# Kernel optimization log

Measured on AMD Instinct MI355X. Metric: run time of the kernel, lower is better.

## Reference

```python
import jax, jax.numpy as jnp
import numpy as np

MARGIN = 0.3
N, D = 8192, 256
NUM_IDS = 1000


def setup_inputs() -> dict:
    key = jax.random.key(0)
    k1, k2 = jax.random.split(key)
    inputs = jax.random.normal(k1, (N, D), dtype=jnp.float32)
    targets = jax.random.randint(k2, (N,), 0, NUM_IDS, dtype=jnp.int64)
    return {"inputs": inputs, "targets": targets}


def reference(inputs, targets):
    # sim_mat[i, j] = <x_i, x_j>
    sim = jnp.matmul(inputs, inputs.T)  # [n, n]
    same = targets[:, None] == targets[None, :]  # [n, n] bool
    # positives: same label AND sim < 1 (note: strict; diagonal included only if ||x||^2 < 1)
    pos_mask = same & (sim < 1.0)
    # negatives: different label AND sim > margin
    neg_mask = (~same) & (sim > MARGIN)
    pos_loss = jnp.sum(jnp.where(pos_mask, 1.0 - sim, 0.0), axis=1)  # [n]
    neg_loss = jnp.sum(jnp.where(neg_mask, sim, 0.0), axis=1)  # [n]
    n = inputs.shape[0]
    return jnp.sum(pos_loss + neg_loss) / n
```

## Files before the change

kernel.cpp:

```cpp
#include <hip/hip_runtime.h>
#include <hip/hip_bf16.h>


#define MARGINF 0.3f

typedef __attribute__((ext_vector_type(8))) short short8x;
typedef __attribute__((ext_vector_type(16))) float f32x16;

__device__ __forceinline__ unsigned short f2bf(float f) {
    unsigned int u = __float_as_uint(f);
    unsigned int r = (u + 0x7fffu + ((u >> 16) & 1u)) >> 16;
    return (unsigned short)r;
}

__global__ void __launch_bounds__(256) convert_k(const float* __restrict__ x,
                                                 unsigned short* __restrict__ xb) {
    int u = blockIdx.x * 256 + threadIdx.x;
    int lane = u & 63;
    int ks   = (u >> 6) & 15;
    int r32  = u >> 10;
    int row  = r32 * 32 + (lane & 31);
    int col  = ks * 16 + (lane >> 5) * 8;
    const float4* src = reinterpret_cast<const float4*>(x + (size_t)row * 256 + col);
    float4 a = src[0];
    float4 b = src[1];
    short8x o;
    o[0] = (short)f2bf(a.x); o[1] = (short)f2bf(a.y);
    o[2] = (short)f2bf(a.z); o[3] = (short)f2bf(a.w);
    o[4] = (short)f2bf(b.x); o[5] = (short)f2bf(b.y);
    o[6] = (short)f2bf(b.z); o[7] = (short)f2bf(b.w);
    reinterpret_cast<short8x*>(xb)[u] = o;
}

__global__ void __launch_bounds__(256, 3) gemm_loss_k(const unsigned short* __restrict__ xb,
                                                      const int* __restrict__ tg,
                                                      double* __restrict__ partials) {
    const int p = blockIdx.x;
    int bi = (int)(64.5f - sqrtf(64.5f * 64.5f - 2.0f * (float)p));
    if (bi < 0) bi = 0;
    if (bi > 63) bi = 63;
    while (bi > 0 && (bi * (129 - bi)) / 2 > p) --bi;
    while (((bi + 1) * (128 - bi)) / 2 <= p) ++bi;
    const int bj = bi + (p - (bi * (129 - bi)) / 2);

    __shared__ int lti[128];
    __shared__ int ltj[128];
    __shared__ float redbuf[4];

    const int tid  = threadIdx.x;
    const int lane = tid & 63;
    const int wid  = tid >> 6;
    const int wr   = wid >> 1;
    const int wc   = wid & 1;

    if (tid < 128)       lti[tid]        = tg[bi * 128 + tid];
    else                 ltj[tid - 128]  = tg[bj * 128 + (tid - 128)];
    __syncthreads();

    const short8x* xf = reinterpret_cast<const short8x*>(xb);
    const int aIdx = ((bi * 4 + wr * 2) << 10) + lane;
    const int bIdx = ((bj * 4 + wc * 2) << 10) + lane;

    f32x16 acc00 = {}, acc01 = {}, acc10 = {}, acc11 = {};

    short8x a0 = xf[aIdx];
    short8x a1 = xf[aIdx + 1024];
    short8x b0 = xf[bIdx];
    short8x b1 = xf[bIdx + 1024];

#pragma unroll
    for (int ks = 0; ks < 16; ++ks) {
        short8x na0, na1, nb0, nb1;
        if (ks < 15) {
            const int o = (ks + 1) * 64;
            na0 = xf[aIdx + o];
            na1 = xf[aIdx + 1024 + o];
            nb0 = xf[bIdx + o];
            nb1 = xf[bIdx + 1024 + o];
        }
        acc00 = __builtin_amdgcn_mfma_f32_32x32x16_bf16(a0, b0, acc00, 0, 0, 0);
        acc01 = __builtin_amdgcn_mfma_f32_32x32x16_bf16(a0, b1, acc01, 0, 0, 0);
        acc10 = __builtin_amdgcn_mfma_f32_32x32x16_bf16(a1, b0, acc10, 0, 0, 0);
        acc11 = __builtin_amdgcn_mfma_f32_32x32x16_bf16(a1, b1, acc11, 0, 0, 0);
        if (ks < 15) { a0 = na0; a1 = na1; b0 = nb0; b1 = nb1; }
    }

    const int hi4 = (lane >> 5) * 4;
    const int col_l = lane & 31;
    int tjv[2];
#pragma unroll
    for (int fn = 0; fn < 2; ++fn) tjv[fn] = ltj[wc * 64 + fn * 32 + col_l];

    float lsum = 0.f;
    const f32x16* accs[4] = { &acc00, &acc01, &acc10, &acc11 };

    if (bi != bj) {
#pragma unroll
        for (int fm = 0; fm < 2; ++fm) {
#pragma unroll
            for (int fn = 0; fn < 2; ++fn) {
                const f32x16& A = *accs[fm * 2 + fn];
                const int tj = tjv[fn];
#pragma unroll
                for (int r = 0; r < 16; ++r) {
                    const int row_l = (r & 3) + 8 * (r >> 2) + hi4;
                    const int ti = lti[wr * 64 + fm * 32 + row_l];
                    const float s = A[r];
                    const float posv = fmaxf(1.0f - s, 0.0f);
                    const float negv = (s > MARGINF) ? s : 0.0f;
                    lsum += (ti == tj) ? posv : negv;
                }
            }
        }
        lsum *= 2.0f;
    } else {
#pragma unroll
        for (int fm = 0; fm < 2; ++fm) {
#pragma unroll
            for (int fn = 0; fn < 2; ++fn) {
                const f32x16& A = *accs[fm * 2 + fn];
                const int tj = tjv[fn];
                const int cl = wc * 64 + fn * 32 + col_l;
#pragma unroll
                for (int r = 0; r < 16; ++r) {
                    const int row_l = (r & 3) + 8 * (r >> 2) + hi4;
                    const int rl = wr * 64 + fm * 32 + row_l;
                    const int ti = lti[rl];
                    const float s = A[r];
                    const float posv = fmaxf(1.0f - s, 0.0f);
                    const float negv = (s > MARGINF) ? s : 0.0f;
                    const float c = (ti == tj) ? posv : negv;
                    const float w = (cl > rl) ? 2.0f : ((cl == rl) ? 1.0f : 0.0f);
                    lsum += w * c;
                }
            }
        }
    }

#pragma unroll
    for (int mask = 1; mask < 64; mask <<= 1) lsum += __shfl_xor(lsum, mask, 64);
    if (lane == 0) redbuf[wid] = lsum;
    __syncthreads();
    if (tid == 0)
        partials[p] = (double)(redbuf[0] + redbuf[1] + redbuf[2] + redbuf[3]);
}

__global__ void __launch_bounds__(256) finalize_k(const double* __restrict__ partials,
                                                  float* __restrict__ out) {
    double s = 0.0;
    for (int i = threadIdx.x; i < 2080; i += 256) s += partials[i];
#pragma unroll
    for (int mask = 1; mask < 64; mask <<= 1) s += __shfl_xor(s, mask, 64);
    __shared__ double red[4];
    const int wid = threadIdx.x >> 6;
    if ((threadIdx.x & 63) == 0) red[wid] = s;
    __syncthreads();
    if (threadIdx.x == 0)
        out[0] = (float)((red[0] + red[1] + red[2] + red[3]) / 8192.0);
}

extern "C" void kernel_launch(void* const* d_in, const int* in_sizes, int n_in,
                              void* d_out, int out_size, void* d_ws, size_t ws_size,
                              hipStream_t stream) {
    (void)in_sizes; (void)n_in; (void)out_size; (void)ws_size;
    const float* x  = (const float*)d_in[0];
    const int*   tg = (const int*)d_in[1];
    float* out = (float*)d_out;

    double* partials   = (double*)d_ws;
    unsigned short* xb = (unsigned short*)((char*)d_ws + 32768);

    convert_k<<<1024, 256, 0, stream>>>(x, xb);
    gemm_loss_k<<<2080, 256, 0, stream>>>(xb, tg, partials);
    finalize_k<<<1, 256, 0, stream>>>(partials, out);
}
```

Before: 89.26 us.

## Stage GEMM operands through swizzled LDS with triple-buffered async global-to-LDS loads

The GEMM now stages A and B tiles through a three-deep LDS ring buffer using global_load_lds direct copies with an XOR swizzle. Waves read their MFMA fragments from LDS instead of each wave loading its own fragments from global memory in a prepacked layout. The convert kernel is simplified to a plain row-major bf16 conversion. This shares operand loads across waves and overlaps memory with MFMA work, at the cost of 48KB of LDS per block, which may limit the three-blocks-per-CU occupancy, plus extra barriers.

```diff
diff --git a/kernel.cpp b/kernel.cpp
--- a/kernel.cpp
+++ b/kernel.cpp
@@ -15,21 +15,16 @@
 
 __global__ void __launch_bounds__(256) convert_k(const float* __restrict__ x,
                                                  unsigned short* __restrict__ xb) {
-    int u = blockIdx.x * 256 + threadIdx.x;
-    int lane = u & 63;
-    int ks   = (u >> 6) & 15;
-    int r32  = u >> 10;
-    int row  = r32 * 32 + (lane & 31);
-    int col  = ks * 16 + (lane >> 5) * 8;
-    const float4* src = reinterpret_cast<const float4*>(x + (size_t)row * 256 + col);
-    float4 a = src[0];
-    float4 b = src[1];
+    int i = blockIdx.x * 256 + threadIdx.x;
+    const float4* p = reinterpret_cast<const float4*>(x) + (size_t)i * 2;
+    float4 a = p[0];
+    float4 b = p[1];
     short8x o;
     o[0] = (short)f2bf(a.x); o[1] = (short)f2bf(a.y);
     o[2] = (short)f2bf(a.z); o[3] = (short)f2bf(a.w);
     o[4] = (short)f2bf(b.x); o[5] = (short)f2bf(b.y);
     o[6] = (short)f2bf(b.z); o[7] = (short)f2bf(b.w);
-    reinterpret_cast<short8x*>(xb)[u] = o;
+    reinterpret_cast<short8x*>(xb)[i] = o;
 }
 
 __global__ void __launch_bounds__(256, 3) gemm_loss_k(const unsigned short* __restrict__ xb,
@@ -43,6 +38,7 @@
     while (((bi + 1) * (128 - bi)) / 2 <= p) ++bi;
     const int bj = bi + (p - (bi * (129 - bi)) / 2);
 
+    __shared__ __align__(16) char ldsb[3 * 16384];
     __shared__ int lti[128];
     __shared__ int ltj[128];
     __shared__ float redbuf[4];
@@ -57,36 +53,92 @@
     else                 ltj[tid - 128]  = tg[bj * 128 + (tid - 128)];
     __syncthreads();
 
-    const short8x* xf = reinterpret_cast<const short8x*>(xb);
-    const int aIdx = ((bi * 4 + wr * 2) << 10) + lane;
-    const int bIdx = ((bj * 4 + wc * 2) << 10) + lane;
+    const char* aBase = (const char*)(xb + (size_t)bi * 128 * 256);
+    const char* bBase = (const char*)(xb + (size_t)bj * 128 * 256);
+
+    const int srow0  = wid * 16 + (lane >> 2);
+    const int schunk = (((lane & 3) ^ ((lane >> 3) & 3))) << 4;
+
+    const int l31 = lane & 31;
+    const int hi  = lane >> 5;
+    const int swz = (l31 >> 1) & 3;
+    int offA[2][2], offB[2][2];
+#pragma unroll
+    for (int fm = 0; fm < 2; ++fm)
+#pragma unroll
+        for (int ks = 0; ks < 2; ++ks)
+            offA[fm][ks] = (wr * 64 + fm * 32 + l31) * 64 + ((((ks << 1) | hi) ^ swz) << 4);
+#pragma unroll
+    for (int fn = 0; fn < 2; ++fn)
+#pragma unroll
+        for (int ks = 0; ks < 2; ++ks)
+            offB[fn][ks] = 8192 + (wc * 64 + fn * 32 + l31) * 64 + ((((ks << 1) | hi) ^ swz) << 4);
 
     f32x16 acc00 = {}, acc01 = {}, acc10 = {}, acc11 = {};
 
-    short8x a0 = xf[aIdx];
-    short8x a1 = xf[aIdx + 1024];
-    short8x b0 = xf[bIdx];
-    short8x b1 = xf[bIdx + 1024];
-
-#pragma unroll
-    for (int ks = 0; ks < 16; ++ks) {
-        short8x na0, na1, nb0, nb1;
-        if (ks < 15) {
-            const int o = (ks + 1) * 64;
-            na0 = xf[aIdx + o];
-            na1 = xf[aIdx + 1024 + o];
-            nb0 = xf[bIdx + o];
-            nb1 = xf[bIdx + 1024 + o];
-        }
-        acc00 = __builtin_amdgcn_mfma_f32_32x32x16_bf16(a0, b0, acc00, 0, 0, 0);
-        acc01 = __builtin_amdgcn_mfma_f32_32x32x16_bf16(a0, b1, acc01, 0, 0, 0);
-        acc10 = __builtin_amdgcn_mfma_f32_32x32x16_bf16(a1, b0, acc10, 0, 0, 0);
-        acc11 = __builtin_amdgcn_mfma_f32_32x32x16_bf16(a1, b1, acc11, 0, 0, 0);
-        if (ks < 15) { a0 = na0; a1 = na1; b0 = nb0; b1 = nb1; }
-    }
-
-    const int hi4 = (lane >> 5) * 4;
-    const int col_l = lane & 31;
+#define STAGE_KT(BUF, T) do {                                                        \
+    _Pragma("unroll")                                                                \
+    for (int i_ = 0; i_ < 2; ++i_) {                                                 \
+        const int r_ = i_ * 64 + srow0;                                              \
+        const char* sa_ = aBase + (size_t)r_ * 512 + (T) * 64 + schunk;              \
+        const char* sb_ = bBase + (size_t)r_ * 512 + (T) * 64 + schunk;              \
+        __builtin_amdgcn_global_load_lds(                                            \
+            (const __attribute__((address_space(1))) unsigned int*)sa_,              \
+            (__attribute__((address_space(3))) unsigned int*)(ldsb + (BUF) * 16384 + i_ * 4096 + wid * 1024), \
+            16, 0, 0);                                                               \
+        __builtin_amdgcn_global_load_lds(                                            \
+            (const __attribute__((address_space(1))) unsigned int*)sb_,              \
+            (__attribute__((address_space(3))) unsigned int*)(ldsb + (BUF) * 16384 + 8192 + i_ * 4096 + wid * 1024), \
+            16, 0, 0);                                                               \
+    }                                                                                \
+} while (0)
+
+#define GEMM_ITER(T, BUF, VMSTR, DOSTAGE) do {                                       \
+    asm volatile("s_waitcnt vmcnt(" VMSTR ")" ::: "memory");                         \
+    __builtin_amdgcn_s_barrier();                     \
+    const char* lb_ = ldsb + (BUF) * 16384;                                          \
+    short8x a0k0 = *(const short8x*)(lb_ + offA[0][0]);                              \
+    short8x a1k0 = *(const short8x*)(lb_ + offA[1][0]);                              \
+    short8x b0k0 = *(const short8x*)(lb_ + offB[0][0]);                              \
+    short8x b1k0 = *(const short8x*)(lb_ + offB[1][0]);                              \
+    short8x a0k1 = *(const short8x*)(lb_ + offA[0][1]);                              \
+    short8x a1k1 = *(const short8x*)(lb_ + offA[1][1]);                              \
+    short8x b0k1 = *(const short8x*)(lb_ + offB[0][1]);                              \
+    short8x b1k1 = *(const short8x*)(lb_ + offB[1][1]);                              \
+    asm volatile("s_waitcnt lgkmcnt(0)" ::: "memory");                               \
+    __builtin_amdgcn_sched_barrier(0);                                               \
+    __builtin_amdgcn_s_barrier();                    \
+    if (DOSTAGE) STAGE_KT(BUF, (T) + 3);                    \
+    __builtin_amdgcn_s_setprio(1);                                                   \
+    acc00 = __builtin_amdgcn_mfma_f32_32x32x16_bf16(a0k0, b0k0, acc00, 0, 0, 0);     \
+    acc01 = __builtin_amdgcn_mfma_f32_32x32x16_bf16(a0k0, b1k0, acc01, 0, 0, 0);     \
+    acc10 = __builtin_amdgcn_mfma_f32_32x32x16_bf16(a1k0, b0k0, acc10, 0, 0, 0);     \
+    acc11 = __builtin_amdgcn_mfma_f32_32x32x16_bf16(a1k0, b1k0, acc11, 0, 0, 0);     \
+    acc00 = __builtin_amdgcn_mfma_f32_32x32x16_bf16(a0k1, b0k1, acc00, 0, 0, 0);     \
+    acc01 = __builtin_amdgcn_mfma_f32_32x32x16_bf16(a0k1, b1k1, acc01, 0, 0, 0);     \
+    acc10 = __builtin_amdgcn_mfma_f32_32x32x16_bf16(a1k1, b0k1, acc10, 0, 0, 0);     \
+    acc11 = __builtin_amdgcn_mfma_f32_32x32x16_bf16(a1k1, b1k1, acc11, 0, 0, 0);     \
+    __builtin_amdgcn_s_setprio(0);                                                   \
+} while (0)
+
+    STAGE_KT(0, 0);
+    STAGE_KT(1, 1);
+    STAGE_KT(2, 2);
+
+    GEMM_ITER(0, 0, "8", 1);
+    GEMM_ITER(1, 1, "8", 1);
+    GEMM_ITER(2, 2, "8", 1);
+    GEMM_ITER(3, 0, "8", 1);
+    GEMM_ITER(4, 1, "8", 1);
+    GEMM_ITER(5, 2, "8", 0);
+    GEMM_ITER(6, 0, "4", 0);
+    GEMM_ITER(7, 1, "0", 0);
+
+#undef GEMM_ITER
+#undef STAGE_KT
+
+    const int hi4 = hi * 4;
+    const int col_l = l31;
     int tjv[2];
 #pragma unroll
     for (int fn = 0; fn < 2; ++fn) tjv[fn] = ltj[wc * 64 + fn * 32 + col_l];
```

Result: no change. 89.50 us (+0.3%).

## Split loss into label-free negative sum plus per-label same-class correction

Applied to the files above, without the earlier changes.

The GEMM epilogue now treats every pair as a negative, summing sim where sim > margin, with no label lookups. A new binning pass groups row indices by label, and a per-label MFMA kernel recomputes same-label pairs to add the positive term and subtract the wrongly counted negative term. The GEMM tile also grows to 256x128, launched as two halves per tile pair, with a block-index swizzle. This removes the label loads and branches from the large epilogue at the cost of three extra small launches and atomics. Groups are capped at 64 members, which would silently truncate larger classes.

```diff
diff --git a/kernel.cpp b/kernel.cpp
--- a/kernel.cpp
+++ b/kernel.cpp
@@ -32,19 +32,20 @@
     reinterpret_cast<short8x*>(xb)[u] = o;
 }
 
-__global__ void __launch_bounds__(256, 3) gemm_loss_k(const unsigned short* __restrict__ xb,
-                                                      const int* __restrict__ tg,
+__global__ void __launch_bounds__(256, 2) gemm_loss_k(const unsigned short* __restrict__ xb,
                                                       double* __restrict__ partials) {
-    const int p = blockIdx.x;
-    int bi = (int)(64.5f - sqrtf(64.5f * 64.5f - 2.0f * (float)p));
+    const int praw  = blockIdx.x;
+    const int p_lin = (praw & 7) * 132 + (praw >> 3);
+    const int s     = p_lin >> 1;
+    const int h     = p_lin & 1;
+
+    int bi = (int)(32.5f - sqrtf(32.5f * 32.5f - 2.0f * (float)s));
     if (bi < 0) bi = 0;
-    if (bi > 63) bi = 63;
-    while (bi > 0 && (bi * (129 - bi)) / 2 > p) --bi;
-    while (((bi + 1) * (128 - bi)) / 2 <= p) ++bi;
-    const int bj = bi + (p - (bi * (129 - bi)) / 2);
-
-    __shared__ int lti[128];
-    __shared__ int ltj[128];
+    if (bi > 31) bi = 31;
+    while (bi > 0 && (bi * (65 - bi)) / 2 > s) --bi;
+    while (((bi + 1) * (64 - bi)) / 2 <= s) ++bi;
+    const int bj = bi + (s - (bi * (65 - bi)) / 2);
+
     __shared__ float redbuf[4];
 
     const int tid  = threadIdx.x;
@@ -53,102 +54,157 @@
     const int wr   = wid >> 1;
     const int wc   = wid & 1;
 
-    if (tid < 128)       lti[tid]        = tg[bi * 128 + tid];
-    else                 ltj[tid - 128]  = tg[bj * 128 + (tid - 128)];
-    __syncthreads();
-
     const short8x* xf = reinterpret_cast<const short8x*>(xb);
-    const int aIdx = ((bi * 4 + wr * 2) << 10) + lane;
-    const int bIdx = ((bj * 4 + wc * 2) << 10) + lane;
-
-    f32x16 acc00 = {}, acc01 = {}, acc10 = {}, acc11 = {};
+    const int aIdx = ((bi * 8 + wr * 4) * 16) * 64 + lane;
+    const int bIdx = ((bj * 8 + h * 4 + wc * 2) * 16) * 64 + lane;
+
+    f32x16 acc[4][2] = {};
 
     short8x a0 = xf[aIdx];
     short8x a1 = xf[aIdx + 1024];
+    short8x a2 = xf[aIdx + 2048];
+    short8x a3 = xf[aIdx + 3072];
     short8x b0 = xf[bIdx];
     short8x b1 = xf[bIdx + 1024];
 
 #pragma unroll
     for (int ks = 0; ks < 16; ++ks) {
-        short8x na0, na1, nb0, nb1;
+        short8x na0, na1, na2, na3, nb0, nb1;
         if (ks < 15) {
             const int o = (ks + 1) * 64;
             na0 = xf[aIdx + o];
             na1 = xf[aIdx + 1024 + o];
+            na2 = xf[aIdx + 2048 + o];
+            na3 = xf[aIdx + 3072 + o];
             nb0 = xf[bIdx + o];
             nb1 = xf[bIdx + 1024 + o];
         }
-        acc00 = __builtin_amdgcn_mfma_f32_32x32x16_bf16(a0, b0, acc00, 0, 0, 0);
-        acc01 = __builtin_amdgcn_mfma_f32_32x32x16_bf16(a0, b1, acc01, 0, 0, 0);
-        acc10 = __builtin_amdgcn_mfma_f32_32x32x16_bf16(a1, b0, acc10, 0, 0, 0);
-        acc11 = __builtin_amdgcn_mfma_f32_32x32x16_bf16(a1, b1, acc11, 0, 0, 0);
-        if (ks < 15) { a0 = na0; a1 = na1; b0 = nb0; b1 = nb1; }
+        acc[0][0] = __builtin_amdgcn_mfma_f32_32x32x16_bf16(a0, b0, acc[0][0], 0, 0, 0);
+        acc[0][1] = __builtin_amdgcn_mfma_f32_32x32x16_bf16(a0, b1, acc[0][1], 0, 0, 0);
+        acc[1][0] = __builtin_amdgcn_mfma_f32_32x32x16_bf16(a1, b0, acc[1][0], 0, 0, 0);
+        acc[1][1] = __builtin_amdgcn_mfma_f32_32x32x16_bf16(a1, b1, acc[1][1], 0, 0, 0);
+        acc[2][0] = __builtin_amdgcn_mfma_f32_32x32x16_bf16(a2, b0, acc[2][0], 0, 0, 0);
+        acc[2][1] = __builtin_amdgcn_mfma_f32_32x32x16_bf16(a2, b1, acc[2][1], 0, 0, 0);
+        acc[3][0] = __builtin_amdgcn_mfma_f32_32x32x16_bf16(a3, b0, acc[3][0], 0, 0, 0);
+        acc[3][1] = __builtin_amdgcn_mfma_f32_32x32x16_bf16(a3, b1, acc[3][1], 0, 0, 0);
+        if (ks < 15) { a0 = na0; a1 = na1; a2 = na2; a3 = na3; b0 = nb0; b1 = nb1; }
     }
 
-    const int hi4 = (lane >> 5) * 4;
-    const int col_l = lane & 31;
-    int tjv[2];
-#pragma unroll
-    for (int fn = 0; fn < 2; ++fn) tjv[fn] = ltj[wc * 64 + fn * 32 + col_l];
-
     float lsum = 0.f;
-    const f32x16* accs[4] = { &acc00, &acc01, &acc10, &acc11 };
-
-    if (bi != bj) {
-#pragma unroll
-        for (int fm = 0; fm < 2; ++fm) {
-#pragma unroll
-            for (int fn = 0; fn < 2; ++fn) {
-                const f32x16& A = *accs[fm * 2 + fn];
-                const int tj = tjv[fn];
-#pragma unroll
-                for (int r = 0; r < 16; ++r) {
-                    const int row_l = (r & 3) + 8 * (r >> 2) + hi4;
-                    const int ti = lti[wr * 64 + fm * 32 + row_l];
-                    const float s = A[r];
-                    const float posv = fmaxf(1.0f - s, 0.0f);
-                    const float negv = (s > MARGINF) ? s : 0.0f;
-                    lsum += (ti == tj) ? posv : negv;
-                }
-            }
-        }
-        lsum *= 2.0f;
-    } else {
-#pragma unroll
-        for (int fm = 0; fm < 2; ++fm) {
-#pragma unroll
-            for (int fn = 0; fn < 2; ++fn) {
-                const f32x16& A = *accs[fm * 2 + fn];
-                const int tj = tjv[fn];
-                const int cl = wc * 64 + fn * 32 + col_l;
-#pragma unroll
-                for (int r = 0; r < 16; ++r) {
-                    const int row_l = (r & 3) + 8 * (r >> 2) + hi4;
-                    const int rl = wr * 64 + fm * 32 + row_l;
-                    const int ti = lti[rl];
-                    const float s = A[r];
-                    const float posv = fmaxf(1.0f - s, 0.0f);
-                    const float negv = (s > MARGINF) ? s : 0.0f;
-                    const float c = (ti == tj) ? posv : negv;
-                    const float w = (cl > rl) ? 2.0f : ((cl == rl) ? 1.0f : 0.0f);
-                    lsum += w * c;
-                }
-            }
-        }
-    }
+#pragma unroll
+    for (int fm = 0; fm < 4; ++fm)
+#pragma unroll
+        for (int fn = 0; fn < 2; ++fn)
+#pragma unroll
+            for (int r = 0; r < 16; ++r) {
+                const float v = acc[fm][fn][r];
+                lsum += (v > MARGINF) ? v : 0.0f;
+            }
+    if (bi != bj) lsum *= 2.0f;
 
 #pragma unroll
     for (int mask = 1; mask < 64; mask <<= 1) lsum += __shfl_xor(lsum, mask, 64);
     if (lane == 0) redbuf[wid] = lsum;
     __syncthreads();
     if (tid == 0)
-        partials[p] = (double)(redbuf[0] + redbuf[1] + redbuf[2] + redbuf[3]);
+        partials[blockIdx.x] = (double)(redbuf[0] + redbuf[1] + redbuf[2] + redbuf[3]);
+}
+
+__global__ void __launch_bounds__(256) zero_k(int* __restrict__ gcnt) {
+    int i = blockIdx.x * 256 + threadIdx.x;
+    if (i < 1000) gcnt[i] = 0;
+}
+
+__global__ void __launch_bounds__(256) bin_k(const int* __restrict__ tg,
+                                             int* __restrict__ gcnt,
+                                             int* __restrict__ glist) {
+    int i = blockIdx.x * 256 + threadIdx.x;
+    int l = tg[i];
+    int q = atomicAdd(&gcnt[l], 1);
+    if (q < 64) glist[l * 64 + q] = i;
+}
+
+__global__ void __launch_bounds__(256) pairsum_k(const unsigned short* __restrict__ xb,
+                                                 const int* __restrict__ gcnt,
+                                                 const int* __restrict__ glist,
+                                                 double* __restrict__ partials2) {
+    const int wid  = threadIdx.x >> 6;
+    const int lane = threadIdx.x & 63;
+    const int lbl  = blockIdx.x * 4 + wid;
+    const int l31  = lane & 31;
+    const int hi   = lane >> 5;
+
+    __shared__ double dred[4];
+
+    int c = gcnt[lbl];
+    if (c > 64) c = 64;
+    float lsum = 0.f;
+
+    const short8x* xf = reinterpret_cast<const short8x*>(xb);
+
+    {
+        const int ridx = (l31 < c) ? glist[lbl * 64 + l31] : 0;
+        const int fbase = (ridx >> 5) * 16;
+        const int fl    = hi * 32 + (ridx & 31);
+        f32x16 acc = {};
+#pragma unroll
+        for (int ks = 0; ks < 16; ++ks) {
+            short8x f = xf[(fbase + ks) * 64 + fl];
+            acc = __builtin_amdgcn_mfma_f32_32x32x16_bf16(f, f, acc, 0, 0, 0);
+        }
+#pragma unroll
+        for (int r = 0; r < 16; ++r) {
+            const int row_l = (r & 3) + 8 * (r >> 2) + hi * 4;
+            if (row_l < c && l31 < c) {
+                const float sv = acc[r];
+                const float posv = (sv < 1.0f) ? (1.0f - sv) : 0.0f;
+                const float negv = (sv > MARGINF) ? sv : 0.0f;
+                lsum += posv - negv;
+            }
+        }
+    }
+
+    if (c > 32) {
+#pragma unroll 1
+        for (int q = 1; q < 4; ++q) {
+            const int qa = q >> 1, qb = q & 1;
+            const int ia = qa * 32 + l31, ib = qb * 32 + l31;
+            const int ridxA = (ia < c) ? glist[lbl * 64 + ia] : 0;
+            const int ridxB = (ib < c) ? glist[lbl * 64 + ib] : 0;
+            const int fbA = (ridxA >> 5) * 16, flA = hi * 32 + (ridxA & 31);
+            const int fbB = (ridxB >> 5) * 16, flB = hi * 32 + (ridxB & 31);
+            f32x16 acc = {};
+#pragma unroll
+            for (int ks = 0; ks < 16; ++ks) {
+                short8x fa = xf[(fbA + ks) * 64 + flA];
+                short8x fb = xf[(fbB + ks) * 64 + flB];
+                acc = __builtin_amdgcn_mfma_f32_32x32x16_bf16(fa, fb, acc, 0, 0, 0);
+            }
+#pragma unroll
+            for (int r = 0; r < 16; ++r) {
+                const int row_l = (r & 3) + 8 * (r >> 2) + hi * 4;
+                if (qa * 32 + row_l < c && qb * 32 + l31 < c) {
+                    const float sv = acc[r];
+                    const float posv = (sv < 1.0f) ? (1.0f - sv) : 0.0f;
+                    const float negv = (sv > MARGINF) ? sv : 0.0f;
+                    lsum += posv - negv;
+                }
+            }
+        }
+    }
+
+#pragma unroll
+    for (int mask = 1; mask < 64; mask <<= 1) lsum += __shfl_xor(lsum, mask, 64);
+    if (lane == 0) dred[wid] = (double)lsum;
+    __syncthreads();
+    if (threadIdx.x == 0)
+        partials2[blockIdx.x] = dred[0] + dred[1] + dred[2] + dred[3];
 }
 
 __global__ void __launch_bounds__(256) finalize_k(const double* __restrict__ partials,
                                                   float* __restrict__ out) {
     double s = 0.0;
-    for (int i = threadIdx.x; i < 2080; i += 256) s += partials[i];
+    for (int i = threadIdx.x; i < 1306; i += 256) s += partials[i];
 #pragma unroll
     for (int mask = 1; mask < 64; mask <<= 1) s += __shfl_xor(s, mask, 64);
     __shared__ double red[4];
@@ -168,9 +224,15 @@
     float* out = (float*)d_out;
 
     double* partials   = (double*)d_ws;
-    unsigned short* xb = (unsigned short*)((char*)d_ws + 32768);
+    double* partials2  = (double*)d_ws + 1056;
+    int*    gcnt       = (int*)((char*)d_ws + 12288);
+    int*    glist      = (int*)((char*)d_ws + 16384);
+    unsigned short* xb = (unsigned short*)((char*)d_ws + 294912);
 
     convert_k<<<1024, 256, 0, stream>>>(x, xb);
-    gemm_loss_k<<<2080, 256, 0, stream>>>(xb, tg, partials);
+    zero_k<<<4, 256, 0, stream>>>(gcnt);
+    bin_k<<<32, 256, 0, stream>>>(tg, gcnt, glist);
+    gemm_loss_k<<<1056, 256, 0, stream>>>(xb, partials);
+    pairsum_k<<<250, 256, 0, stream>>>(xb, gcnt, glist, partials2);
     finalize_k<<<1, 256, 0, stream>>>(partials, out);
 }
```

New measurement: 104.9 us. +17.5%, slower.
